# Performance work log

Hardware: AMD Instinct MI355X
Metric: run time of the kernel (lower is better)

## Reference

```python
import jax, jax.numpy as jnp
import numpy as np

B, N, M, D = 4, 1024, 1024, 64


def setup_inputs() -> dict:
    key = jax.random.key(0)
    k1, k2 = jax.random.split(key)
    lhs = jax.random.normal(k1, (B, N, D), dtype=jnp.float32)
    rhs = jax.random.normal(k2, (B, M, D), dtype=jnp.float32)
    return {"lhs": lhs, "rhs": rhs}


def reference(lhs, rhs):
    # SAD similarity: -sum_d |lhs[b,n,d] - rhs[b,m,d]|  -> [B, N, M]
    # Faithful to the torch module's broadcasted abs-diff reduction.
    diff = lhs[:, :, None, :] - rhs[:, None, :, :]  # [B, N, M, D]
    similarity = -jnp.abs(diff).sum(axis=-1)        # [B, N, M]
    return similarity
```

## Files before the change

kernel.cpp:

```cpp
#include <hip/hip_runtime.h>

#define BB 4
#define NN 1024
#define MM 1024
#define DD 64
#define TILE 64
#define PAD 68

__global__ __launch_bounds__(256, 4)
void SADSimilarity_38706245272206_kernel(const float* __restrict__ lhs,
                                         const float* __restrict__ rhs,
                                         float* __restrict__ out) {
    __shared__ float lt[TILE * PAD];
    __shared__ float rt[TILE * PAD];

    const int b  = blockIdx.z;
    const int n0 = blockIdx.y * TILE;
    const int m0 = blockIdx.x * TILE;
    const int tid = threadIdx.x;

    const float* lbase = lhs + (size_t)b * NN * DD + (size_t)n0 * DD;
    const float* rbase = rhs + (size_t)b * MM * DD + (size_t)m0 * DD;

    #pragma unroll
    for (int p = 0; p < 4; ++p) {
        int e   = tid + p * 256;
        int row = e >> 4;
        int q   = (e & 15) << 2;
        float4 lv = *(const float4*)(lbase + row * DD + q);
        float4 rv = *(const float4*)(rbase + row * DD + q);
        *(float4*)(&lt[row * PAD + q]) = lv;
        *(float4*)(&rt[row * PAD + q]) = rv;
    }
    __syncthreads();

    const int tx = tid & 15;
    const int ty = tid >> 4;

    float acc[4][4];
    #pragma unroll
    for (int i = 0; i < 4; ++i)
        #pragma unroll
        for (int j = 0; j < 4; ++j) acc[i][j] = 0.0f;

    #pragma unroll 2
    for (int dq = 0; dq < DD / 4; ++dq) {
        float4 l[4], r[4];
        #pragma unroll
        for (int i = 0; i < 4; ++i)
            l[i] = *(const float4*)(&lt[(ty + 16 * i) * PAD + dq * 4]);
        #pragma unroll
        for (int j = 0; j < 4; ++j)
            r[j] = *(const float4*)(&rt[(tx + 16 * j) * PAD + dq * 4]);
        #pragma unroll
        for (int i = 0; i < 4; ++i)
            #pragma unroll
            for (int j = 0; j < 4; ++j) {
                acc[i][j] += fabsf(l[i].x - r[j].x);
                acc[i][j] += fabsf(l[i].y - r[j].y);
                acc[i][j] += fabsf(l[i].z - r[j].z);
                acc[i][j] += fabsf(l[i].w - r[j].w);
            }
    }

    float* obase = out + (size_t)b * NN * MM + (size_t)n0 * MM + m0;
    #pragma unroll
    for (int i = 0; i < 4; ++i) {
        int row = ty + 16 * i;
        #pragma unroll
        for (int j = 0; j < 4; ++j) {
            obase[(size_t)row * MM + tx + 16 * j] = -acc[i][j];
        }
    }
}

extern "C" void kernel_launch(void* const* d_in, const int* in_sizes, int n_in,
                              void* d_out, int out_size, void* d_ws, size_t ws_size,
                              hipStream_t stream) {
    const float* lhs = (const float*)d_in[0];
    const float* rhs = (const float*)d_in[1];
    float* out = (float*)d_out;

    dim3 grid(MM / TILE, NN / TILE, BB);
    dim3 block(256, 1, 1);
    SADSimilarity_38706245272206_kernel<<<grid, block, 0, stream>>>(lhs, rhs, out);
}
```

Before: 78.63 us.

## Keep rhs rows in registers and broadcast lhs rows from shared memory

Each thread now loads one full rhs row (64 floats) into registers, and only the lhs tile is staged in shared memory. Each wave then walks 16 lhs rows, reading them as same-address broadcast LDS loads and writing one output column per lane with coalesced stores. This is meant to remove the rhs shared-memory staging and the strided, uncoalesced output stores. In exchange it loses the 4x4 register blocking, so it issues more LDS loads per output. The inner loop is only partially unrolled, so the register array rr[q] is indexed dynamically and may spill to scratch memory.

```diff
diff --git a/kernel.cpp b/kernel.cpp
--- a/kernel.cpp
+++ b/kernel.cpp
@@ -5,72 +5,48 @@
 #define MM 1024
 #define DD 64
 #define TILE 64
-#define PAD 68
+
 
 __global__ __launch_bounds__(256, 4)
 void SADSimilarity_38706245272206_kernel(const float* __restrict__ lhs,
                                          const float* __restrict__ rhs,
                                          float* __restrict__ out) {
-    __shared__ float lt[TILE * PAD];
-    __shared__ float rt[TILE * PAD];
+    __shared__ float lt[TILE * DD];
 
-    const int b  = blockIdx.z;
-    const int n0 = blockIdx.y * TILE;
-    const int m0 = blockIdx.x * TILE;
-    const int tid = threadIdx.x;
+    const int b    = blockIdx.z;
+    const int n0   = blockIdx.y * TILE;
+    const int m0   = blockIdx.x * TILE;
+    const int tid  = threadIdx.x;
+    const int lane = tid & 63;
+    const int w    = tid >> 6;
 
-    const float* lbase = lhs + (size_t)b * NN * DD + (size_t)n0 * DD;
-    const float* rbase = rhs + (size_t)b * MM * DD + (size_t)m0 * DD;
+    const float* rrow = rhs + ((size_t)(b * MM + m0 + lane)) * DD;
+    float4 rr[16];
+    #pragma unroll
+    for (int q = 0; q < 16; ++q) rr[q] = *(const float4*)(rrow + 4 * q);
 
+    const float* lbase = lhs + ((size_t)(b * NN + n0)) * DD;
     #pragma unroll
     for (int p = 0; p < 4; ++p) {
-        int e   = tid + p * 256;
-        int row = e >> 4;
-        int q   = (e & 15) << 2;
-        float4 lv = *(const float4*)(lbase + row * DD + q);
-        float4 rv = *(const float4*)(rbase + row * DD + q);
-        *(float4*)(&lt[row * PAD + q]) = lv;
-        *(float4*)(&rt[row * PAD + q]) = rv;
+        int idx = tid + p * 256;
+        *(float4*)(&lt[idx * 4]) = *(const float4*)(lbase + idx * 4);
     }
     __syncthreads();
 
-    const int tx = tid & 15;
-    const int ty = tid >> 4;
+    float* obase = out + ((size_t)(b * NN + n0 + w * 16)) * MM + m0 + lane;
 
-    float acc[4][4];
-    #pragma unroll
-    for (int i = 0; i < 4; ++i)
-        #pragma unroll
-        for (int j = 0; j < 4; ++j) acc[i][j] = 0.0f;
-
-    #pragma unroll 2
-    for (int dq = 0; dq < DD / 4; ++dq) {
-        float4 l[4], r[4];
-        #pragma unroll
-        for (int i = 0; i < 4; ++i)
-            l[i] = *(const float4*)(&lt[(ty + 16 * i) * PAD + dq * 4]);
-        #pragma unroll
-        for (int j = 0; j < 4; ++j)
-            r[j] = *(const float4*)(&rt[(tx + 16 * j) * PAD + dq * 4]);
-        #pragma unroll
-        for (int i = 0; i < 4; ++i)
-            #pragma unroll
-            for (int j = 0; j < 4; ++j) {
-                acc[i][j] += fabsf(l[i].x - r[j].x);
-                acc[i][j] += fabsf(l[i].y - r[j].y);
-                acc[i][j] += fabsf(l[i].z - r[j].z);
-                acc[i][j] += fabsf(l[i].w - r[j].w);
-            }
-    }
-
-    float* obase = out + (size_t)b * NN * MM + (size_t)n0 * MM + m0;
-    #pragma unroll
-    for (int i = 0; i < 4; ++i) {
-        int row = ty + 16 * i;
-        #pragma unroll
-        for (int j = 0; j < 4; ++j) {
-            obase[(size_t)row * MM + tx + 16 * j] = -acc[i][j];
+    for (int n = 0; n < 16; ++n) {
+        const float* Lr = &lt[(w * 16 + n) * DD];
+        float a0 = 0.f, a1 = 0.f, a2 = 0.f, a3 = 0.f;
+        #pragma unroll 4
+        for (int q = 0; q < 16; ++q) {
+            float4 lv = *(const float4*)(Lr + 4 * q);
+            a0 += fabsf(rr[q].x - lv.x);
+            a1 += fabsf(rr[q].y - lv.y);
+            a2 += fabsf(rr[q].z - lv.z);
+            a3 += fabsf(rr[q].w - lv.w);
         }
+        obase[(size_t)n * MM] = -((a0 + a1) + (a2 + a3));
     }
 }
 
```

Result: slower. 204.1 us (+159.6%).
